# Performance work log

Hardware: AMD Instinct MI355X
Metric: run time of the kernel (lower is better)

## Reference

```python
import jax, jax.numpy as jnp
import numpy as np

B, T, F, U = 16, 400, 512, 1024
EPS = 1e-3  # Keras BatchNormalization default epsilon


def _run_lstm(x, k, r, b):
    # x: [B,T,F], k: [F,4U], r: [U,4U], b: [4U]  (Keras gate order: i,f,g,o)
    xw = jnp.einsum('btf,fg->btg', x, k) + b  # precompute input projections [B,T,4U]

    def step(carry, xw_t):
        h, c = carry
        z = xw_t + h @ r
        i, f, g, o = jnp.split(z, 4, axis=-1)
        c = jax.nn.sigmoid(f) * c + jax.nn.sigmoid(i) * jnp.tanh(g)
        h = jax.nn.sigmoid(o) * jnp.tanh(c)
        return (h, c), h

    zeros = jnp.zeros((x.shape[0], r.shape[0]), x.dtype)
    _, hs = jax.lax.scan(step, (zeros, zeros), jnp.swapaxes(xw, 0, 1))
    return jnp.swapaxes(hs, 0, 1)  # [B,T,U]


def setup_inputs() -> dict:
    key = jax.random.key(0)
    ks = jax.random.split(key, 6)
    s_in = 1.0 / np.sqrt(F)
    s_rec = 1.0 / np.sqrt(U)
    return {
        'x': jax.random.normal(ks[0], (B, T, F), jnp.float32),
        'k_fwd': jax.random.normal(ks[1], (F, 4 * U), jnp.float32) * s_in,
        'r_fwd': jax.random.normal(ks[2], (U, 4 * U), jnp.float32) * s_rec,
        'b_fwd': jnp.zeros((4 * U,), jnp.float32),
        'k_bwd': jax.random.normal(ks[3], (F, 4 * U), jnp.float32) * s_in,
        'r_bwd': jax.random.normal(ks[4], (U, 4 * U), jnp.float32) * s_rec,
        'b_bwd': jnp.zeros((4 * U,), jnp.float32),
        'gamma': jnp.ones((2 * U,), jnp.float32),
        'beta': jnp.zeros((2 * U,), jnp.float32),
        'mov_mean': jnp.zeros((2 * U,), jnp.float32),
        'mov_var': jnp.ones((2 * U,), jnp.float32),
    }


def reference(x, k_fwd, r_fwd, b_fwd, k_bwd, r_bwd, b_bwd, gamma, beta, mov_mean, mov_var):
    # Bidirectional LSTM, merge_mode='concat'
    h_f = _run_lstm(x, k_fwd, r_fwd, b_fwd)
    h_b = _run_lstm(x[:, ::-1, :], k_bwd, r_bwd, b_bwd)[:, ::-1, :]
    h = jnp.concatenate([h_f, h_b], axis=-1)  # [B,T,2U]
    # SequenceBatchNorm, inference path (training=False): moving statistics
    inv = gamma * jax.lax.rsqrt(mov_var + EPS)
    return h * inv + (beta - mov_mean * inv)
```

## Files before the change

kernel.cpp:

```cpp
#include <hip/hip_runtime.h>
#include <hip/hip_fp16.h>

#define B_  16
#define T_  400
#define F_  512
#define U_  1024
#define G4_ 4096
#define NBLK 256

typedef __attribute__((ext_vector_type(8))) short short8;
typedef __attribute__((ext_vector_type(4))) float f32x4;

__device__ __forceinline__ unsigned bf16bits(float f) {
  unsigned u = __float_as_uint(f);
  return (u + 0x7fffu + ((u >> 16) & 1u)) >> 16;
}
__device__ __forceinline__ float sigm(float x)   { return 1.f/(1.f + __expf(-x)); }
__device__ __forceinline__ float tanh_f(float x) { return 2.f/(1.f + __expf(-2.f*x)) - 1.f; }

__device__ __forceinline__ void ast(unsigned* p, unsigned v) {
  __hip_atomic_store(p, v, __ATOMIC_RELAXED, __HIP_MEMORY_SCOPE_AGENT);
}

__device__ __forceinline__ uint4 ald4_wait(const unsigned* p) {
  uint4 v;
  asm volatile("global_load_dwordx4 %0, %1, off sc0 sc1\n\t"
               "s_waitcnt vmcnt(0)"
               : "=&v"(v) : "v"(p) : "memory");
  return v;
}
__device__ __forceinline__ void load_frag8(const unsigned* p,
    uint4& q0, uint4& q1, uint4& q2, uint4& q3,
    uint4& q4, uint4& q5, uint4& q6, uint4& q7) {
  asm volatile(
    "global_load_dwordx4 %0, %[a], off sc0 sc1\n\t"
    "global_load_dwordx4 %1, %[a], off offset:64 sc0 sc1\n\t"
    "global_load_dwordx4 %2, %[a], off offset:128 sc0 sc1\n\t"
    "global_load_dwordx4 %3, %[a], off offset:192 sc0 sc1\n\t"
    "global_load_dwordx4 %4, %[a], off offset:256 sc0 sc1\n\t"
    "global_load_dwordx4 %5, %[a], off offset:320 sc0 sc1\n\t"
    "global_load_dwordx4 %6, %[a], off offset:384 sc0 sc1\n\t"
    "global_load_dwordx4 %7, %[a], off offset:448 sc0 sc1\n\t"
    "s_waitcnt vmcnt(0)"
    : "=&v"(q0), "=&v"(q1), "=&v"(q2), "=&v"(q3),
      "=&v"(q4), "=&v"(q5), "=&v"(q6), "=&v"(q7)
    : [a] "v"(p)
    : "memory");
}

__global__ __launch_bounds__(256) void preconv_x(
    const float* __restrict__ X, unsigned short* __restrict__ Xbf)
{
  const size_t base = ((size_t)blockIdx.x*256 + threadIdx.x) * 8;
  const float4 v0 = *reinterpret_cast<const float4*>(&X[base]);
  const float4 v1 = *reinterpret_cast<const float4*>(&X[base + 4]);
  short8 t;
  t[0]=(short)bf16bits(v0.x); t[1]=(short)bf16bits(v0.y);
  t[2]=(short)bf16bits(v0.z); t[3]=(short)bf16bits(v0.w);
  t[4]=(short)bf16bits(v1.x); t[5]=(short)bf16bits(v1.y);
  t[6]=(short)bf16bits(v1.z); t[7]=(short)bf16bits(v1.w);
  *reinterpret_cast<short8*>(&Xbf[base]) = t;
}

__global__ __launch_bounds__(256) void transp_k(
    const float* __restrict__ Kf, const float* __restrict__ Kb,
    unsigned short* __restrict__ KbfT)
{
  __shared__ float tile[64][68];
  const int k0 = blockIdx.x * 64;
  const int n0 = blockIdx.y * 64;
  const int dir = blockIdx.z;
  const float* Km = dir ? Kb : Kf;
  const int tid = threadIdx.x;

  #pragma unroll
  for (int i = 0; i < 4; ++i) {
    const int kr = (tid >> 4) + i*16;
    const int nc = (tid & 15) * 4;
    const float4 v = *reinterpret_cast<const float4*>(&Km[(size_t)(k0+kr)*G4_ + n0 + nc]);
    tile[kr][nc+0] = v.x; tile[kr][nc+1] = v.y;
    tile[kr][nc+2] = v.z; tile[kr][nc+3] = v.w;
  }
  __syncthreads();
  const int n  = tid >> 2;
  const int kc = (tid & 3) * 16;
  short8 a, b;
  #pragma unroll
  for (int j = 0; j < 8; ++j) a[j] = (short)bf16bits(tile[kc + j][n]);
  #pragma unroll
  for (int j = 0; j < 8; ++j) b[j] = (short)bf16bits(tile[kc + 8 + j][n]);
  unsigned short* out = &KbfT[((size_t)dir*G4_ + n0 + n)*F_ + k0 + kc];
  *reinterpret_cast<short8*>(out)     = a;
  *reinterpret_cast<short8*>(out + 8) = b;
}

__global__ __launch_bounds__(256) void gemm_xw(
    const unsigned short* __restrict__ Xbf,
    const unsigned short* __restrict__ KbfT,
    const float* __restrict__ Bf, const float* __restrict__ Bb,
    __half* __restrict__ xwf, __half* __restrict__ xwb)
{
  const int dir = blockIdx.z;
  const float* bias = dir ? Bb : Bf;
  __half* outp      = dir ? xwb : xwf;
  const unsigned short* Kt = KbfT + (size_t)dir*G4_*F_;
  const int m0 = blockIdx.x * 128;
  const int n0 = blockIdx.y * 128;
  const int tid = threadIdx.x, wid = tid >> 6, lane = tid & 63;
  const int wm = wid >> 1, wn = wid & 1;
  const int arow = lane & 15, kgrp = lane >> 4;

  const unsigned short* ap = &Xbf[(size_t)(m0 + wm*64 + arow)*F_ + kgrp*8];
  const unsigned short* bp = &Kt [(size_t)(n0 + wn*64 + arow)*F_ + kgrp*8];

  f32x4 acc[4][4];
  #pragma unroll
  for (int i = 0; i < 4; ++i)
    #pragma unroll
    for (int j = 0; j < 4; ++j)
      acc[i][j] = (f32x4){0.f,0.f,0.f,0.f};

  #pragma unroll 2
  for (int kk = 0; kk < 16; ++kk) {
    const int ko = kk*32;
    short8 af[4], bf4[4];
    #pragma unroll
    for (int t = 0; t < 4; ++t) {
      af[t]  = *reinterpret_cast<const short8*>(ap + (size_t)t*16*F_ + ko);
      bf4[t] = *reinterpret_cast<const short8*>(bp + (size_t)t*16*F_ + ko);
    }
    #pragma unroll
    for (int mt = 0; mt < 4; ++mt)
      #pragma unroll
      for (int nt = 0; nt < 4; ++nt)
        acc[mt][nt] = __builtin_amdgcn_mfma_f32_16x16x32_bf16(af[mt], bf4[nt], acc[mt][nt], 0, 0, 0);
  }
  #pragma unroll
  for (int mt = 0; mt < 4; ++mt) {
    #pragma unroll
    for (int nt = 0; nt < 4; ++nt) {
      const int n = n0 + wn*64 + nt*16 + arow;
      const float bv = bias[n];
      #pragma unroll
      for (int r = 0; r < 4; ++r) {
        const int m = m0 + wm*64 + mt*16 + kgrp*4 + r;
        outp[(size_t)m*G4_ + n] = __float2half_rn(acc[mt][nt][r] + bv);
      }
    }
  }
}

__global__ __launch_bounds__(256, 1) void lstm_rec(
    const __half* __restrict__ xwf, const __half* __restrict__ xwb,
    const float* __restrict__ Rf, const float* __restrict__ Rb,
    const float* __restrict__ gammav, const float* __restrict__ betav,
    const float* __restrict__ mmean, const float* __restrict__ mvar,
    unsigned* __restrict__ hw2p,
    float* __restrict__ outp)
{
  __shared__ unsigned short r_bf[32*1040];
  __shared__ float z_s[2][4*528];

  const int wg  = blockIdx.x;
  const int dir = wg >> 7;
  const int u0  = (wg & 127) * 8;
  const __half* xw = dir ? xwb : xwf;
  const float*  R  = dir ? Rb  : Rf;
  const int tid  = threadIdx.x;
  const int wid  = tid >> 6;
  const int lane = tid & 63;

  {
    const int c4 = (tid & 7) * 4;
    const int kb = (tid >> 3) * 32;
    const int gcol = ((c4 >> 3) * U_) + u0 + (c4 & 7);
    for (int kk = 0; kk < 32; ++kk) {
      const float4 rv = *reinterpret_cast<const float4*>(&R[(size_t)(kb+kk)*G4_ + gcol]);
      r_bf[(c4+0)*1040 + kb+kk] = (unsigned short)bf16bits(rv.x);
      r_bf[(c4+1)*1040 + kb+kk] = (unsigned short)bf16bits(rv.y);
      r_bf[(c4+2)*1040 + kb+kk] = (unsigned short)bf16bits(rv.z);
      r_bf[(c4+3)*1040 + kb+kk] = (unsigned short)bf16bits(rv.w);
    }
  }

  float inv = 0.f, add = 0.f, cst = 0.f;
  const int gb = tid >> 3, uu = tid & 7;
  if (tid < 128) {
    const int j = dir*U_ + u0 + uu;
    inv = gammav[j] * rsqrtf(mvar[j] + 1e-3f);
    add = betav[j] - mmean[j]*inv;
    if (!(uu & 1))
      ast(&hw2p[(size_t)((0*2 + dir)*16 + gb)*512 + (u0 >> 1) + (uu >> 1)], 1u);
  }
  __syncthreads();

  const int arow = lane & 15;
  const int kgrp = lane >> 4;
  const unsigned short* bc0 = &r_bf[arow*1040 + wid*256];
  const unsigned short* bc1 = &r_bf[(16 + arow)*1040 + wid*256];
  #define LB(P, K) (*reinterpret_cast<const short8*>(&(P)[(K)*32 + kgrp*8]))
  const short8 rb00 = LB(bc0,0), rb01 = LB(bc0,1), rb02 = LB(bc0,2), rb03 = LB(bc0,3);
  const short8 rb04 = LB(bc0,4), rb05 = LB(bc0,5), rb06 = LB(bc0,6), rb07 = LB(bc0,7);
  const short8 rb10 = LB(bc1,0), rb11 = LB(bc1,1), rb12 = LB(bc1,2), rb13 = LB(bc1,3);
  const short8 rb14 = LB(bc1,4), rb15 = LB(bc1,5), rb16 = LB(bc1,6), rb17 = LB(bc1,7);
  #undef LB
  const size_t hfrag_off = (size_t)arow*512 + wid*128 + kgrp*4;
  const size_t samp_off  = (size_t)((lane >> 5)*8)*512 + wid*128 + (lane & 31)*4;

  for (int s = 0; s < T_; ++s) {
    const int tin = dir ? (T_-1-s) : s;

    float xv0=0.f, xv1=0.f, xv2=0.f, xv3=0.f;
    if (tid < 128) {
      const __half* xp = &xw[((size_t)gb*T_ + tin)*G4_ + u0 + uu];
      xv0 = __half2float(xp[0]);    xv1 = __half2float(xp[1024]);
      xv2 = __half2float(xp[2048]); xv3 = __half2float(xp[3072]);
    }

    const unsigned eb = (((unsigned)s >> 1) & 1u) ^ 1u;
    const size_t pbase = (size_t)((s&1)*2 + dir)*8192;
    #define CKB(Q) (((Q.x ^ eb) | (Q.y ^ eb) | (Q.z ^ eb) | (Q.w ^ eb)) & 1u)

    {
      const unsigned* sp = hw2p + pbase + samp_off;
      for (;;) {
        const uint4 t = ald4_wait(sp);
        if (__all((int)(CKB(t) == 0u))) break;
        __builtin_amdgcn_s_sleep(1);
      }
    }

    const unsigned* hgp = hw2p + pbase + hfrag_off;
    uint4 q0,q1,q2,q3,q4,q5,q6,q7;
    for (;;) {
      load_frag8(hgp, q0,q1,q2,q3,q4,q5,q6,q7);
      const unsigned mism = CKB(q0)|CKB(q1)|CKB(q2)|CKB(q3)
                          | CKB(q4)|CKB(q5)|CKB(q6)|CKB(q7);
      if (__all((int)(mism == 0u))) break;
      __builtin_amdgcn_s_sleep(1);
    }
    #undef CKB
    __builtin_amdgcn_sched_barrier(0);

    f32x4 acc0 = {0.f,0.f,0.f,0.f}, acc1 = {0.f,0.f,0.f,0.f};
    #define FRAG(Q, RB0, RB1) { \
      const short8 a = *reinterpret_cast<const short8*>(&Q); \
      acc0 = __builtin_amdgcn_mfma_f32_16x16x32_bf16(a, RB0, acc0, 0, 0, 0); \
      acc1 = __builtin_amdgcn_mfma_f32_16x16x32_bf16(a, RB1, acc1, 0, 0, 0); }
    FRAG(q0, rb00, rb10) FRAG(q1, rb01, rb11)
    FRAG(q2, rb02, rb12) FRAG(q3, rb03, rb13)
    FRAG(q4, rb04, rb14) FRAG(q5, rb05, rb15)
    FRAG(q6, rb06, rb16) FRAG(q7, rb07, rb17)
    #undef FRAG

    {
      const int col = lane & 15, rbase = kgrp*4;
      float* zw = &z_s[s&1][wid*528];
      #pragma unroll
      for (int r = 0; r < 4; ++r) {
        zw[(rbase+r)*33 + col]      = acc0[r];
        zw[(rbase+r)*33 + 16 + col] = acc1[r];
      }
    }
    __syncthreads();

    if (tid < 128) {
      float zi = xv0, zf = xv1, zg = xv2, zo = xv3;
      #pragma unroll
      for (int w = 0; w < 4; ++w) {
        const float* zr = &z_s[s&1][w*528 + gb*33];
        zi += zr[uu]; zf += zr[8+uu]; zg += zr[16+uu]; zo += zr[24+uu];
      }
      const float ig = sigm(zi), fg = sigm(zf), og = sigm(zo);
      const float gg = tanh_f(zg);
      cst = fg*cst + ig*gg;
      const float hv = og * tanh_f(cst);
      const unsigned hvb = bf16bits(hv);
      const unsigned hnb = (unsigned)__shfl_down((int)hvb, 1);
      if (!(uu & 1)) {
        const unsigned sbit = (((unsigned)(s+1) >> 1) & 1u) ^ 1u;
        const unsigned d = ((hvb & ~1u) | sbit) | (hnb << 16);
        ast(&hw2p[(size_t)((((s+1)&1)*2 + dir)*16 + gb)*512 + (u0 >> 1) + (uu >> 1)], d);
      }
      outp[((size_t)gb*T_ + tin)*2048 + dir*U_ + u0 + uu] = hv*inv + add;
    }
  }
}

extern "C" void kernel_launch(void* const* d_in, const int* in_sizes, int n_in,
                              void* d_out, int out_size, void* d_ws, size_t ws_size,
                              hipStream_t stream)
{
  const float* x  = (const float*)d_in[0];
  const float* kf = (const float*)d_in[1];
  const float* rf = (const float*)d_in[2];
  const float* bf = (const float*)d_in[3];
  const float* kb = (const float*)d_in[4];
  const float* rb = (const float*)d_in[5];
  const float* bb = (const float*)d_in[6];
  const float* ga = (const float*)d_in[7];
  const float* be = (const float*)d_in[8];
  const float* mm = (const float*)d_in[9];
  const float* mv = (const float*)d_in[10];
  float* outp = (float*)d_out;

  unsigned* hw2p       = (unsigned*)d_ws;
  unsigned short* Xbf  = (unsigned short*)((char*)d_ws + 262144);
  unsigned short* KbfT = (unsigned short*)((char*)d_ws + 262144 + (size_t)6400*F_*2);
  __half* xwf          = (__half*)((char*)d_ws + 262144 + (size_t)6400*F_*2
                                   + (size_t)2*G4_*F_*2);
  __half* xwb          = xwf + (size_t)6400*G4_;

  hipMemsetAsync(hw2p, 0, 262144, stream);
  preconv_x<<<dim3(1600), dim3(256), 0, stream>>>(x, Xbf);
  transp_k<<<dim3(8, 64, 2), dim3(256), 0, stream>>>(kf, kb, KbfT);
  gemm_xw<<<dim3(50, 32, 2), dim3(256), 0, stream>>>(Xbf, KbfT, bf, bb, xwf, xwb);
  lstm_rec<<<dim3(NBLK), dim3(256), 0, stream>>>(xwf, xwb, rf, rb, ga, be, mm, mv,
                                                 hw2p, outp);
}
```

Baseline: 1.775 ms.

## Halve recurrent LSTM workgroups, each owning sixteen hidden units per direction

The persistent recurrent kernel drops from 256 to 128 workgroups, so each one now holds 64 gate columns of the recurrent matrix in LDS and registers instead of 32. Every wave issues four MFMA chains per k-slice, and all 256 threads run the cell update instead of half of them. The aim is to cut the number of workgroups that must publish and poll the hidden state each timestep, which lowers global synchronisation traffic per step. In exchange each workgroup does twice the MFMA work, holds more registers, and adds an extra barrier per step, which replaces the old double-buffered z array.

```diff
diff --git a/kernel.cpp b/kernel.cpp
--- a/kernel.cpp
+++ b/kernel.cpp
@@ -6,7 +6,6 @@
 #define F_  512
 #define U_  1024
 #define G4_ 4096
-#define NBLK 256
 
 typedef __attribute__((ext_vector_type(8))) short short8;
 typedef __attribute__((ext_vector_type(4))) float f32x4;
@@ -158,12 +157,12 @@
     unsigned* __restrict__ hw2p,
     float* __restrict__ outp)
 {
-  __shared__ unsigned short r_bf[32*1040];
-  __shared__ float z_s[2][4*528];
+  __shared__ unsigned short r_bf[64*1024];
+  __shared__ float z_s[4][16][66];
 
   const int wg  = blockIdx.x;
-  const int dir = wg >> 7;
-  const int u0  = (wg & 127) * 8;
+  const int dir = wg >> 6;
+  const int u0  = (wg & 63) * 16;
   const __half* xw = dir ? xwb : xwf;
   const float*  R  = dir ? Rb  : Rf;
   const int tid  = threadIdx.x;
@@ -171,47 +170,50 @@
   const int lane = tid & 63;
 
   {
-    const int c4 = (tid & 7) * 4;
-    const int kb = (tid >> 3) * 32;
-    const int gcol = ((c4 >> 3) * U_) + u0 + (c4 & 7);
-    for (int kk = 0; kk < 32; ++kk) {
+    const int c4 = (tid & 15) * 4;
+    const int kb = (tid >> 4) * 64;
+    const int gcol = ((c4 >> 4) * U_) + u0 + (c4 & 15);
+    for (int kk = 0; kk < 64; ++kk) {
       const float4 rv = *reinterpret_cast<const float4*>(&R[(size_t)(kb+kk)*G4_ + gcol]);
-      r_bf[(c4+0)*1040 + kb+kk] = (unsigned short)bf16bits(rv.x);
-      r_bf[(c4+1)*1040 + kb+kk] = (unsigned short)bf16bits(rv.y);
-      r_bf[(c4+2)*1040 + kb+kk] = (unsigned short)bf16bits(rv.z);
-      r_bf[(c4+3)*1040 + kb+kk] = (unsigned short)bf16bits(rv.w);
-    }
-  }
-
-  float inv = 0.f, add = 0.f, cst = 0.f;
-  const int gb = tid >> 3, uu = tid & 7;
-  if (tid < 128) {
+      r_bf[(c4+0)*1024 + kb+kk] = (unsigned short)bf16bits(rv.x);
+      r_bf[(c4+1)*1024 + kb+kk] = (unsigned short)bf16bits(rv.y);
+      r_bf[(c4+2)*1024 + kb+kk] = (unsigned short)bf16bits(rv.z);
+      r_bf[(c4+3)*1024 + kb+kk] = (unsigned short)bf16bits(rv.w);
+    }
+  }
+
+  const int gb = tid >> 4, uu = tid & 15;
+  float inv, add, cst = 0.f;
+  {
     const int j = dir*U_ + u0 + uu;
     inv = gammav[j] * rsqrtf(mvar[j] + 1e-3f);
     add = betav[j] - mmean[j]*inv;
     if (!(uu & 1))
-      ast(&hw2p[(size_t)((0*2 + dir)*16 + gb)*512 + (u0 >> 1) + (uu >> 1)], 1u);
+      ast(&hw2p[(size_t)((0*2 + dir)*16 + gb)*512 + ((u0 + uu) >> 1)], 1u);
   }
   __syncthreads();
 
   const int arow = lane & 15;
   const int kgrp = lane >> 4;
-  const unsigned short* bc0 = &r_bf[arow*1040 + wid*256];
-  const unsigned short* bc1 = &r_bf[(16 + arow)*1040 + wid*256];
-  #define LB(P, K) (*reinterpret_cast<const short8*>(&(P)[(K)*32 + kgrp*8]))
-  const short8 rb00 = LB(bc0,0), rb01 = LB(bc0,1), rb02 = LB(bc0,2), rb03 = LB(bc0,3);
-  const short8 rb04 = LB(bc0,4), rb05 = LB(bc0,5), rb06 = LB(bc0,6), rb07 = LB(bc0,7);
-  const short8 rb10 = LB(bc1,0), rb11 = LB(bc1,1), rb12 = LB(bc1,2), rb13 = LB(bc1,3);
-  const short8 rb14 = LB(bc1,4), rb15 = LB(bc1,5), rb16 = LB(bc1,6), rb17 = LB(bc1,7);
+  #define LB(T, KS) (*reinterpret_cast<const short8*>( \
+      &r_bf[((T)*16 + arow)*1024 + wid*256 + (KS)*32 + kgrp*8]))
+  const short8 rb00=LB(0,0), rb01=LB(0,1), rb02=LB(0,2), rb03=LB(0,3),
+               rb04=LB(0,4), rb05=LB(0,5), rb06=LB(0,6), rb07=LB(0,7);
+  const short8 rb10=LB(1,0), rb11=LB(1,1), rb12=LB(1,2), rb13=LB(1,3),
+               rb14=LB(1,4), rb15=LB(1,5), rb16=LB(1,6), rb17=LB(1,7);
+  const short8 rb20=LB(2,0), rb21=LB(2,1), rb22=LB(2,2), rb23=LB(2,3),
+               rb24=LB(2,4), rb25=LB(2,5), rb26=LB(2,6), rb27=LB(2,7);
+  const short8 rb30=LB(3,0), rb31=LB(3,1), rb32=LB(3,2), rb33=LB(3,3),
+               rb34=LB(3,4), rb35=LB(3,5), rb36=LB(3,6), rb37=LB(3,7);
   #undef LB
   const size_t hfrag_off = (size_t)arow*512 + wid*128 + kgrp*4;
-  const size_t samp_off  = (size_t)((lane >> 5)*8)*512 + wid*128 + (lane & 31)*4;
+  const size_t samp_off  = (size_t)((lane >> 4)*4)*512 + wid*128 + (lane & 15)*8;
 
   for (int s = 0; s < T_; ++s) {
     const int tin = dir ? (T_-1-s) : s;
 
-    float xv0=0.f, xv1=0.f, xv2=0.f, xv3=0.f;
-    if (tid < 128) {
+    float xv0, xv1, xv2, xv3;
+    {
       const __half* xp = &xw[((size_t)gb*T_ + tin)*G4_ + u0 + uu];
       xv0 = __half2float(xp[0]);    xv1 = __half2float(xp[1024]);
       xv2 = __half2float(xp[2048]); xv3 = __half2float(xp[3072]);
@@ -243,34 +245,42 @@
     __builtin_amdgcn_sched_barrier(0);
 
     f32x4 acc0 = {0.f,0.f,0.f,0.f}, acc1 = {0.f,0.f,0.f,0.f};
-    #define FRAG(Q, RB0, RB1) { \
+    f32x4 acc2 = {0.f,0.f,0.f,0.f}, acc3 = {0.f,0.f,0.f,0.f};
+    #define FRAG(Q, B0, B1, B2, B3) { \
       const short8 a = *reinterpret_cast<const short8*>(&Q); \
-      acc0 = __builtin_amdgcn_mfma_f32_16x16x32_bf16(a, RB0, acc0, 0, 0, 0); \
-      acc1 = __builtin_amdgcn_mfma_f32_16x16x32_bf16(a, RB1, acc1, 0, 0, 0); }
-    FRAG(q0, rb00, rb10) FRAG(q1, rb01, rb11)
-    FRAG(q2, rb02, rb12) FRAG(q3, rb03, rb13)
-    FRAG(q4, rb04, rb14) FRAG(q5, rb05, rb15)
-    FRAG(q6, rb06, rb16) FRAG(q7, rb07, rb17)
+      acc0 = __builtin_amdgcn_mfma_f32_16x16x32_bf16(a, B0, acc0, 0, 0, 0); \
+      acc1 = __builtin_amdgcn_mfma_f32_16x16x32_bf16(a, B1, acc1, 0, 0, 0); \
+      acc2 = __builtin_amdgcn_mfma_f32_16x16x32_bf16(a, B2, acc2, 0, 0, 0); \
+      acc3 = __builtin_amdgcn_mfma_f32_16x16x32_bf16(a, B3, acc3, 0, 0, 0); }
+    FRAG(q0, rb00, rb10, rb20, rb30) FRAG(q1, rb01, rb11, rb21, rb31)
+    FRAG(q2, rb02, rb12, rb22, rb32) FRAG(q3, rb03, rb13, rb23, rb33)
+    FRAG(q4, rb04, rb14, rb24, rb34) FRAG(q5, rb05, rb15, rb25, rb35)
+    FRAG(q6, rb06, rb16, rb26, rb36) FRAG(q7, rb07, rb17, rb27, rb37)
     #undef FRAG
 
     {
       const int col = lane & 15, rbase = kgrp*4;
-      float* zw = &z_s[s&1][wid*528];
       #pragma unroll
       for (int r = 0; r < 4; ++r) {
-        zw[(rbase+r)*33 + col]      = acc0[r];
-        zw[(rbase+r)*33 + 16 + col] = acc1[r];
+        z_s[wid][rbase+r][col]      = acc0[r];
+        z_s[wid][rbase+r][16 + col] = acc1[r];
+        z_s[wid][rbase+r][32 + col] = acc2[r];
+        z_s[wid][rbase+r][48 + col] = acc3[r];
       }
     }
     __syncthreads();
 
-    if (tid < 128) {
-      float zi = xv0, zf = xv1, zg = xv2, zo = xv3;
-      #pragma unroll
-      for (int w = 0; w < 4; ++w) {
-        const float* zr = &z_s[s&1][w*528 + gb*33];
-        zi += zr[uu]; zf += zr[8+uu]; zg += zr[16+uu]; zo += zr[24+uu];
-      }
+    float zi = xv0, zf = xv1, zg = xv2, zo = xv3;
+    #pragma unroll
+    for (int w = 0; w < 4; ++w) {
+      zi += z_s[w][gb][uu];
+      zf += z_s[w][gb][16 + uu];
+      zg += z_s[w][gb][32 + uu];
+      zo += z_s[w][gb][48 + uu];
+    }
+    __syncthreads();
+
+    {
       const float ig = sigm(zi), fg = sigm(zf), og = sigm(zo);
       const float gg = tanh_f(zg);
       cst = fg*cst + ig*gg;
@@ -280,7 +290,7 @@
       if (!(uu & 1)) {
         const unsigned sbit = (((unsigned)(s+1) >> 1) & 1u) ^ 1u;
         const unsigned d = ((hvb & ~1u) | sbit) | (hnb << 16);
-        ast(&hw2p[(size_t)((((s+1)&1)*2 + dir)*16 + gb)*512 + (u0 >> 1) + (uu >> 1)], d);
+        ast(&hw2p[(size_t)((((s+1)&1)*2 + dir)*16 + gb)*512 + ((u0 + uu) >> 1)], d);
       }
       outp[((size_t)gb*T_ + tin)*2048 + dir*U_ + u0 + uu] = hv*inv + add;
     }
@@ -315,6 +325,6 @@
   preconv_x<<<dim3(1600), dim3(256), 0, stream>>>(x, Xbf);
   transp_k<<<dim3(8, 64, 2), dim3(256), 0, stream>>>(kf, kb, KbfT);
   gemm_xw<<<dim3(50, 32, 2), dim3(256), 0, stream>>>(Xbf, KbfT, bf, bb, xwf, xwb);
-  lstm_rec<<<dim3(NBLK), dim3(256), 0, stream>>>(xwf, xwb, rf, rb, ga, be, mm, mv,
-                                                 hw2p, outp);
-}
+  lstm_rec<<<dim3(128), dim3(256), 0, stream>>>(xwf, xwb, rf, rb, ga, be, mm, mv,
+                                                hw2p, outp);
+}
```

Result: faster. 1.630 ms (-8.2%).

## Cut recurrent LSTM grid to 64 blocks with 32 units per block

Applied to the files above, without the earlier changes.

The persistent recurrent kernel now runs 64 workgroups instead of 256, and each owns 32 hidden units per direction. Each workgroup holds the matching recurrent weights in registers as 8 bf16 fragment tiles and issues 8 MFMAs per k-slice. All 256 threads now do the gate math for two batch rows each. The aim is fewer workgroups taking part in the per-timestep global flag synchronisation, less polling traffic and more work per step on each CU. In exchange each block does four times more MFMA and gate work per step, register pressure rises sharply (64 short8 weight fragments), and an extra __syncthreads is added per step.

```diff
diff --git a/kernel.cpp b/kernel.cpp
--- a/kernel.cpp
+++ b/kernel.cpp
@@ -6,7 +6,6 @@
 #define F_  512
 #define U_  1024
 #define G4_ 4096
-#define NBLK 256
 
 typedef __attribute__((ext_vector_type(8))) short short8;
 typedef __attribute__((ext_vector_type(4))) float f32x4;
@@ -22,12 +21,12 @@
   __hip_atomic_store(p, v, __ATOMIC_RELAXED, __HIP_MEMORY_SCOPE_AGENT);
 }
 
-__device__ __forceinline__ uint4 ald4_wait(const unsigned* p) {
-  uint4 v;
-  asm volatile("global_load_dwordx4 %0, %1, off sc0 sc1\n\t"
+__device__ __forceinline__ void ald4x2_wait(const unsigned* p0, const unsigned* p1,
+                                            uint4& t0, uint4& t1) {
+  asm volatile("global_load_dwordx4 %0, %[a], off sc0 sc1\n\t"
+               "global_load_dwordx4 %1, %[b], off sc0 sc1\n\t"
                "s_waitcnt vmcnt(0)"
-               : "=&v"(v) : "v"(p) : "memory");
-  return v;
+               : "=&v"(t0), "=&v"(t1) : [a] "v"(p0), [b] "v"(p1) : "memory");
 }
 __device__ __forceinline__ void load_frag8(const unsigned* p,
     uint4& q0, uint4& q1, uint4& q2, uint4& q3,
@@ -158,63 +157,75 @@
     unsigned* __restrict__ hw2p,
     float* __restrict__ outp)
 {
-  __shared__ unsigned short r_bf[32*1040];
-  __shared__ float z_s[2][4*528];
+  __shared__ unsigned short r_stage[32*1032];
+  __shared__ float z_s[4][16][132];
 
   const int wg  = blockIdx.x;
-  const int dir = wg >> 7;
-  const int u0  = (wg & 127) * 8;
+  const int dir = wg >> 5;
+  const int u0  = (wg & 31) * 32;
   const __half* xw = dir ? xwb : xwf;
   const float*  R  = dir ? Rb  : Rf;
   const int tid  = threadIdx.x;
   const int wid  = tid >> 6;
   const int lane = tid & 63;
-
+  const int arow = lane & 15;
+  const int kgrp = lane >> 4;
+
+  short8 rbf[8][8];
+  #pragma unroll
+  for (int j = 0; j < 4; ++j) {
+    {
+      const int c4l = (tid & 7) * 4;
+      const int kb  = (tid >> 3) * 32;
+      const int gcol = j*U_ + u0 + c4l;
+      for (int kk = 0; kk < 32; ++kk) {
+        const float4 rv = *reinterpret_cast<const float4*>(&R[(size_t)(kb+kk)*G4_ + gcol]);
+        r_stage[(c4l+0)*1032 + kb+kk] = (unsigned short)bf16bits(rv.x);
+        r_stage[(c4l+1)*1032 + kb+kk] = (unsigned short)bf16bits(rv.y);
+        r_stage[(c4l+2)*1032 + kb+kk] = (unsigned short)bf16bits(rv.z);
+        r_stage[(c4l+3)*1032 + kb+kk] = (unsigned short)bf16bits(rv.w);
+      }
+    }
+    __syncthreads();
+    #pragma unroll
+    for (int tt = 0; tt < 2; ++tt) {
+      const int lc = tt*16 + arow;
+      #pragma unroll
+      for (int ks = 0; ks < 8; ++ks)
+        rbf[2*j + tt][ks] = *reinterpret_cast<const short8*>(
+            &r_stage[lc*1032 + wid*256 + ks*32 + kgrp*8]);
+    }
+    __syncthreads();
+  }
+
+  const int uu = tid & 31, b0 = tid >> 5, b1 = b0 + 8;
+  float inv, add, cst0 = 0.f, cst1 = 0.f;
   {
-    const int c4 = (tid & 7) * 4;
-    const int kb = (tid >> 3) * 32;
-    const int gcol = ((c4 >> 3) * U_) + u0 + (c4 & 7);
-    for (int kk = 0; kk < 32; ++kk) {
-      const float4 rv = *reinterpret_cast<const float4*>(&R[(size_t)(kb+kk)*G4_ + gcol]);
-      r_bf[(c4+0)*1040 + kb+kk] = (unsigned short)bf16bits(rv.x);
-      r_bf[(c4+1)*1040 + kb+kk] = (unsigned short)bf16bits(rv.y);
-      r_bf[(c4+2)*1040 + kb+kk] = (unsigned short)bf16bits(rv.z);
-      r_bf[(c4+3)*1040 + kb+kk] = (unsigned short)bf16bits(rv.w);
-    }
-  }
-
-  float inv = 0.f, add = 0.f, cst = 0.f;
-  const int gb = tid >> 3, uu = tid & 7;
-  if (tid < 128) {
     const int j = dir*U_ + u0 + uu;
     inv = gammav[j] * rsqrtf(mvar[j] + 1e-3f);
     add = betav[j] - mmean[j]*inv;
-    if (!(uu & 1))
-      ast(&hw2p[(size_t)((0*2 + dir)*16 + gb)*512 + (u0 >> 1) + (uu >> 1)], 1u);
+    if (!(uu & 1)) {
+      ast(&hw2p[(size_t)((0*2 + dir)*16 + b0)*512 + ((u0 + uu) >> 1)], 1u);
+      ast(&hw2p[(size_t)((0*2 + dir)*16 + b1)*512 + ((u0 + uu) >> 1)], 1u);
+    }
   }
   __syncthreads();
 
-  const int arow = lane & 15;
-  const int kgrp = lane >> 4;
-  const unsigned short* bc0 = &r_bf[arow*1040 + wid*256];
-  const unsigned short* bc1 = &r_bf[(16 + arow)*1040 + wid*256];
-  #define LB(P, K) (*reinterpret_cast<const short8*>(&(P)[(K)*32 + kgrp*8]))
-  const short8 rb00 = LB(bc0,0), rb01 = LB(bc0,1), rb02 = LB(bc0,2), rb03 = LB(bc0,3);
-  const short8 rb04 = LB(bc0,4), rb05 = LB(bc0,5), rb06 = LB(bc0,6), rb07 = LB(bc0,7);
-  const short8 rb10 = LB(bc1,0), rb11 = LB(bc1,1), rb12 = LB(bc1,2), rb13 = LB(bc1,3);
-  const short8 rb14 = LB(bc1,4), rb15 = LB(bc1,5), rb16 = LB(bc1,6), rb17 = LB(bc1,7);
-  #undef LB
   const size_t hfrag_off = (size_t)arow*512 + wid*128 + kgrp*4;
-  const size_t samp_off  = (size_t)((lane >> 5)*8)*512 + wid*128 + (lane & 31)*4;
+  const size_t samp_off0 = (size_t)(lane >> 3)*512       + wid*128 + (lane & 7)*16;
+  const size_t samp_off1 = (size_t)((lane >> 3) + 8)*512 + wid*128 + (lane & 7)*16;
 
   for (int s = 0; s < T_; ++s) {
     const int tin = dir ? (T_-1-s) : s;
 
-    float xv0=0.f, xv1=0.f, xv2=0.f, xv3=0.f;
-    if (tid < 128) {
-      const __half* xp = &xw[((size_t)gb*T_ + tin)*G4_ + u0 + uu];
-      xv0 = __half2float(xp[0]);    xv1 = __half2float(xp[1024]);
-      xv2 = __half2float(xp[2048]); xv3 = __half2float(xp[3072]);
+    float x0i, x0f, x0g, x0o, x1i, x1f, x1g, x1o;
+    {
+      const __half* xp0 = &xw[((size_t)b0*T_ + tin)*G4_ + u0 + uu];
+      const __half* xp1 = &xw[((size_t)b1*T_ + tin)*G4_ + u0 + uu];
+      x0i = __half2float(xp0[0]);    x0f = __half2float(xp0[1024]);
+      x0g = __half2float(xp0[2048]); x0o = __half2float(xp0[3072]);
+      x1i = __half2float(xp1[0]);    x1f = __half2float(xp1[1024]);
+      x1g = __half2float(xp1[2048]); x1o = __half2float(xp1[3072]);
     }
 
     const unsigned eb = (((unsigned)s >> 1) & 1u) ^ 1u;
@@ -222,10 +233,12 @@
     #define CKB(Q) (((Q.x ^ eb) | (Q.y ^ eb) | (Q.z ^ eb) | (Q.w ^ eb)) & 1u)
 
     {
-      const unsigned* sp = hw2p + pbase + samp_off;
+      const unsigned* sp0 = hw2p + pbase + samp_off0;
+      const unsigned* sp1 = hw2p + pbase + samp_off1;
       for (;;) {
-        const uint4 t = ald4_wait(sp);
-        if (__all((int)(CKB(t) == 0u))) break;
+        uint4 t0, t1;
+        ald4x2_wait(sp0, sp1, t0, t1);
+        if (__all((int)((CKB(t0) | CKB(t1)) == 0u))) break;
         __builtin_amdgcn_s_sleep(1);
       }
     }
@@ -242,47 +255,62 @@
     #undef CKB
     __builtin_amdgcn_sched_barrier(0);
 
-    f32x4 acc0 = {0.f,0.f,0.f,0.f}, acc1 = {0.f,0.f,0.f,0.f};
-    #define FRAG(Q, RB0, RB1) { \
+    f32x4 acc[8];
+    #pragma unroll
+    for (int t = 0; t < 8; ++t) acc[t] = (f32x4){0.f,0.f,0.f,0.f};
+    #define FRAGK(Q, KS) { \
       const short8 a = *reinterpret_cast<const short8*>(&Q); \
-      acc0 = __builtin_amdgcn_mfma_f32_16x16x32_bf16(a, RB0, acc0, 0, 0, 0); \
-      acc1 = __builtin_amdgcn_mfma_f32_16x16x32_bf16(a, RB1, acc1, 0, 0, 0); }
-    FRAG(q0, rb00, rb10) FRAG(q1, rb01, rb11)
-    FRAG(q2, rb02, rb12) FRAG(q3, rb03, rb13)
-    FRAG(q4, rb04, rb14) FRAG(q5, rb05, rb15)
-    FRAG(q6, rb06, rb16) FRAG(q7, rb07, rb17)
-    #undef FRAG
+      _Pragma("unroll") \
+      for (int t = 0; t < 8; ++t) \
+        acc[t] = __builtin_amdgcn_mfma_f32_16x16x32_bf16(a, rbf[t][KS], acc[t], 0, 0, 0); }
+    FRAGK(q0, 0) FRAGK(q1, 1) FRAGK(q2, 2) FRAGK(q3, 3)
+    FRAGK(q4, 4) FRAGK(q5, 5) FRAGK(q6, 6) FRAGK(q7, 7)
+    #undef FRAGK
 
     {
       const int col = lane & 15, rbase = kgrp*4;
-      float* zw = &z_s[s&1][wid*528];
       #pragma unroll
-      for (int r = 0; r < 4; ++r) {
-        zw[(rbase+r)*33 + col]      = acc0[r];
-        zw[(rbase+r)*33 + 16 + col] = acc1[r];
-      }
+      for (int t = 0; t < 8; ++t)
+        #pragma unroll
+        for (int r = 0; r < 4; ++r)
+          z_s[wid][rbase+r][t*16 + col] = acc[t][r];
     }
     __syncthreads();
 
-    if (tid < 128) {
-      float zi = xv0, zf = xv1, zg = xv2, zo = xv3;
-      #pragma unroll
-      for (int w = 0; w < 4; ++w) {
-        const float* zr = &z_s[s&1][w*528 + gb*33];
-        zi += zr[uu]; zf += zr[8+uu]; zg += zr[16+uu]; zo += zr[24+uu];
-      }
-      const float ig = sigm(zi), fg = sigm(zf), og = sigm(zo);
-      const float gg = tanh_f(zg);
-      cst = fg*cst + ig*gg;
-      const float hv = og * tanh_f(cst);
-      const unsigned hvb = bf16bits(hv);
-      const unsigned hnb = (unsigned)__shfl_down((int)hvb, 1);
+    float z0i = x0i, z0f = x0f, z0g = x0g, z0o = x0o;
+    float z1i = x1i, z1f = x1f, z1g = x1g, z1o = x1o;
+    #pragma unroll
+    for (int w = 0; w < 4; ++w) {
+      z0i += z_s[w][b0][uu];      z1i += z_s[w][b1][uu];
+      z0f += z_s[w][b0][32 + uu]; z1f += z_s[w][b1][32 + uu];
+      z0g += z_s[w][b0][64 + uu]; z1g += z_s[w][b1][64 + uu];
+      z0o += z_s[w][b0][96 + uu]; z1o += z_s[w][b1][96 + uu];
+    }
+    __syncthreads();
+
+    {
+      const float ig0 = sigm(z0i), fg0 = sigm(z0f), og0 = sigm(z0o);
+      const float gg0 = tanh_f(z0g);
+      cst0 = fg0*cst0 + ig0*gg0;
+      const float hv0 = og0 * tanh_f(cst0);
+      const float ig1 = sigm(z1i), fg1 = sigm(z1f), og1 = sigm(z1o);
+      const float gg1 = tanh_f(z1g);
+      cst1 = fg1*cst1 + ig1*gg1;
+      const float hv1 = og1 * tanh_f(cst1);
+      const unsigned hvb0 = bf16bits(hv0);
+      const unsigned hvb1 = bf16bits(hv1);
+      const unsigned hnb0 = (unsigned)__shfl_down((int)hvb0, 1);
+      const unsigned hnb1 = (unsigned)__shfl_down((int)hvb1, 1);
       if (!(uu & 1)) {
         const unsigned sbit = (((unsigned)(s+1) >> 1) & 1u) ^ 1u;
-        const unsigned d = ((hvb & ~1u) | sbit) | (hnb << 16);
-        ast(&hw2p[(size_t)((((s+1)&1)*2 + dir)*16 + gb)*512 + (u0 >> 1) + (uu >> 1)], d);
+        const unsigned d0 = ((hvb0 & ~1u) | sbit) | (hnb0 << 16);
+        const unsigned d1 = ((hvb1 & ~1u) | sbit) | (hnb1 << 16);
+        const size_t nb = (size_t)(((s+1)&1)*2 + dir)*8192;
+        ast(&hw2p[nb + (size_t)b0*512 + ((u0 + uu) >> 1)], d0);
+        ast(&hw2p[nb + (size_t)b1*512 + ((u0 + uu) >> 1)], d1);
       }
-      outp[((size_t)gb*T_ + tin)*2048 + dir*U_ + u0 + uu] = hv*inv + add;
+      outp[((size_t)b0*T_ + tin)*2048 + dir*U_ + u0 + uu] = hv0*inv + add;
+      outp[((size_t)b1*T_ + tin)*2048 + dir*U_ + u0 + uu] = hv1*inv + add;
     }
   }
 }
@@ -315,6 +343,6 @@
   preconv_x<<<dim3(1600), dim3(256), 0, stream>>>(x, Xbf);
   transp_k<<<dim3(8, 64, 2), dim3(256), 0, stream>>>(kf, kb, KbfT);
   gemm_xw<<<dim3(50, 32, 2), dim3(256), 0, stream>>>(Xbf, KbfT, bf, bb, xwf, xwb);
-  lstm_rec<<<dim3(NBLK), dim3(256), 0, stream>>>(xwf, xwb, rf, rb, ga, be, mm, mv,
-                                                 hw2p, outp);
-}
+  lstm_rec<<<dim3(64), dim3(256), 0, stream>>>(xwf, xwb, rf, rb, ga, be, mm, mv,
+                                               hw2p, outp);
+}
```

Result: faster. 1.613 ms (median of 2 runs) (-9.1%).
